# Performance work log

Hardware: AMD Instinct MI355X
Metric: run time of the kernel (lower is better)

The kernel has to match this reference:

```python
import jax, jax.numpy as jnp
import numpy as np

B, N, HID = 4, 16384, 512
H, M = 8, 32          # num_heads, num_slices
D = HID // H          # head_dim = 64


def setup_inputs() -> dict:
    key = jax.random.key(0)
    ks = jax.random.split(key, 8)
    std = 0.02
    return {
        "x": jax.random.normal(ks[0], (B, N, HID), jnp.float32),
        # Linear weights stored as [in, out] (y = x @ W + b)
        "wkv_w": jax.random.normal(ks[1], (HID, 2 * HID), jnp.float32) * std,
        "wkv_b": jnp.zeros((2 * HID,), jnp.float32),
        "wtq": jax.random.normal(ks[2], (H, M, D), jnp.float32) * std,
        "alpha": jnp.ones((H,), jnp.float32),
        "qkv_w": jax.random.normal(ks[3], (HID, 3 * HID), jnp.float32) * std,
        "out_w": jax.random.normal(ks[4], (HID, HID), jnp.float32) * std,
        "out_b": jnp.zeros((HID,), jnp.float32),
    }


def _split_heads(t):  # [b, n, h*d] -> [b, h, n, d]
    b, n, _ = t.shape
    return t.reshape(b, n, H, D).transpose(0, 2, 1, 3)


def _mha(q, k, v):
    scale = q.shape[-1] ** -0.5
    dots = jnp.einsum('bhqd,bhkd->bhqk', q, k) * scale
    attn = jax.nn.softmax(dots, axis=-1)
    out = jnp.einsum('bhqk,bhkd->bhqd', attn, v)
    return out, attn


def reference(x, wkv_w, wkv_b, wtq, alpha, qkv_w, out_w, out_b):
    kv = x @ wkv_w + wkv_b                      # [b, n, 2*hid]
    xk, xv = kv[..., :HID], kv[..., HID:]
    xk = _split_heads(xk)                       # [b, h, n, d]
    xv = _split_heads(xv)

    # slot/slice cross-attention: softmax over the slice axis m (axis=-2)
    slice_scores = jnp.einsum('hmd,bhnd->bhmn', wtq, xk)
    slice_weights = jax.nn.softmax(slice_scores * alpha[None, :, None, None], axis=-2)
    slice_token = jnp.einsum('bhmn,bhnd->bhmd', slice_weights, xv)
    slice_token = slice_token / (slice_weights.sum(axis=-1, keepdims=True) + 1e-5)
    slice_token = slice_token.transpose(0, 2, 1, 3).reshape(B, M, HID)  # b m (h d)

    # small inner MHA over the m=32 slices
    qkv = slice_token @ qkv_w                   # [b, m, 3*hid]
    q_t = _split_heads(qkv[..., :HID])
    k_t = _split_heads(qkv[..., HID:2 * HID])
    v_t = _split_heads(qkv[..., 2 * HID:])
    out_token, attn_weights = _mha(q_t, k_t, v_t)

    # scatter slice outputs back to n positions
    out = jnp.einsum('bhmd,bhmn->bhnd', out_token, slice_weights)
    out = out.transpose(0, 2, 1, 3).reshape(B, N, HID)  # b n (h d)
    out = out @ out_w + out_b
    return out, slice_weights, alpha, jnp.zeros((H, M), jnp.float32), attn_weights
```

## Files before the change

### kernel.cpp

```cpp
#include <hip/hip_runtime.h>

#define B_ 4
#define N_ 16384
#define HID_ 512
#define H_ 8
#define M_ 32
#define D_ 64

typedef __attribute__((ext_vector_type(8))) short short8;
typedef __attribute__((ext_vector_type(4))) float f32x4;

__device__ __forceinline__ short f2bf(float f) {
    unsigned u = __float_as_uint(f);
    u += 0x7fffu + ((u >> 16) & 1u);
    return (short)(u >> 16);
}
__device__ __forceinline__ float bf2f(short s) {
    return __uint_as_float(((unsigned)(unsigned short)s) << 16);
}
__device__ __forceinline__ unsigned pack2(float a, float b) {
    return (unsigned)(unsigned short)f2bf(a) | ((unsigned)(unsigned short)f2bf(b) << 16);
}
__device__ __forceinline__ void gl_lds16(const short* g, short* l) {
    __builtin_amdgcn_global_load_lds((const __attribute__((address_space(1))) unsigned*)g,
                                     (__attribute__((address_space(3))) unsigned*)l, 16, 0, 0);
}

__global__ void k_misc(const float* __restrict__ alpha, float* __restrict__ a_out,
                       float* __restrict__ z_out, const float* __restrict__ wtq,
                       short* __restrict__ wtq_bf) {
    int i = blockIdx.x * 256 + threadIdx.x;
    wtq_bf[i] = f2bf(wtq[i]);
    if (blockIdx.x == 0) {
        int t = threadIdx.x;
        if (t < H_) a_out[t] = alpha[t];
        z_out[t] = 0.f;
    }
}

__global__ void k_cvt(const float* __restrict__ src, short* __restrict__ dst) {
    int i = blockIdx.x * 256 + threadIdx.x;
    const f32x4* s = (const f32x4*)(src) + (size_t)i * 2;
    f32x4 a = s[0], b = s[1];
    short8 o;
    o[0] = f2bf(a[0]); o[1] = f2bf(a[1]); o[2] = f2bf(a[2]); o[3] = f2bf(a[3]);
    o[4] = f2bf(b[0]); o[5] = f2bf(b[1]); o[6] = f2bf(b[2]); o[7] = f2bf(b[3]);
    ((short8*)dst)[i] = o;
}

__global__ __launch_bounds__(256)
void k_wt(const float* __restrict__ w, short* __restrict__ wt) {
    __shared__ float ls[64][65];
    const int t = threadIdx.x;
    const int n0 = blockIdx.x * 64, k0 = blockIdx.y * 64;
#pragma unroll
    for (int p = 0; p < 16; ++p) {
        int idx = p * 256 + t;
        int kk = idx >> 6, nn = idx & 63;
        ls[kk][nn] = w[(size_t)(k0 + kk) * 1024 + n0 + nn];
    }
    __syncthreads();
#pragma unroll
    for (int p = 0; p < 16; ++p) {
        int idx = p * 256 + t;
        int nn = idx >> 6, kk = idx & 63;
        wt[(size_t)(n0 + nn) * 512 + k0 + kk] = f2bf(ls[kk][nn]);
    }
}

template <bool OUT_BF16>
__global__ __launch_bounds__(256, 2)
void mfma_gemm(const short* __restrict__ A, const short* __restrict__ Bt,
               const float* __restrict__ bias, void* __restrict__ Cv,
               int K, int Ncols, int b_stride, int rows_per_b, int lgx) {
    __shared__ short As[128 * 32];
    __shared__ short Bs[128 * 32];
    const int t = threadIdx.x;
    const int nwg = gridDim.x * gridDim.y;
    int id = blockIdx.y * gridDim.x + blockIdx.x;
    id = (id & 7) * (nwg >> 3) + (id >> 3);
    const int col0 = (id & ((1 << lgx) - 1)) * 128;
    const int row0 = (id >> lgx) * 128;
    const short* Bblk = Bt;
    if (b_stride) Bblk += (size_t)(row0 / rows_per_b) * (size_t)b_stride;

    const int r_a = t >> 2;
    const int c_a = (t & 3) << 3;
    const short* Ap = A + (size_t)(row0 + r_a) * K + c_a;
    const short* Bp = Bblk + (size_t)(col0 + r_a) * K + c_a;
    short* As0 = &As[t << 3];
    short* Bs0 = &Bs[t << 3];
    const size_t rowskip = (size_t)64 * K;

    const int w = t >> 6;
    const int L = t & 63;
    const int wm = (w >> 1) << 6;
    const int wn = (w & 1) << 6;
    const int lm = L & 15;
    const int lq = L >> 4;

    f32x4 acc[4][4];
#pragma unroll
    for (int i = 0; i < 4; ++i)
#pragma unroll
        for (int j = 0; j < 4; ++j) acc[i][j] = (f32x4){0.f, 0.f, 0.f, 0.f};

    for (int k0 = 0; k0 < K; k0 += 32) {
        gl_lds16(Ap + k0, As0);
        gl_lds16(Ap + k0 + rowskip, As0 + 2048);
        gl_lds16(Bp + k0, Bs0);
        gl_lds16(Bp + k0 + rowskip, Bs0 + 2048);
        __syncthreads();
        short8 af[4], bfr[4];
#pragma unroll
        for (int i = 0; i < 4; ++i)
            af[i] = *(const short8*)&As[((wm + (i << 4) + lm) << 5) + (lq << 3)];
#pragma unroll
        for (int j = 0; j < 4; ++j)
            bfr[j] = *(const short8*)&Bs[((wn + (j << 4) + lm) << 5) + (lq << 3)];
#pragma unroll
        for (int i = 0; i < 4; ++i)
#pragma unroll
            for (int j = 0; j < 4; ++j)
                acc[i][j] = __builtin_amdgcn_mfma_f32_16x16x32_bf16(af[i], bfr[j], acc[i][j], 0, 0, 0);
        __syncthreads();
    }
#pragma unroll
    for (int i = 0; i < 4; ++i) {
#pragma unroll
        for (int j = 0; j < 4; ++j) {
            const int gr = row0 + wm + (i << 4) + (lq << 2);
            const int gc = col0 + wn + (j << 4) + lm;
            const float bv = bias[gc];
#pragma unroll
            for (int r = 0; r < 4; ++r) {
                float v = acc[i][j][r] + bv;
                if constexpr (OUT_BF16)
                    ((short*)Cv)[(size_t)(gr + r) * Ncols + gc] = f2bf(v);
                else
                    ((float*)Cv)[(size_t)(gr + r) * Ncols + gc] = v;
            }
        }
    }
}

__global__ __launch_bounds__(256, 4)
void k_score(const short* __restrict__ kv, const short* __restrict__ wtq_bf,
             const float* __restrict__ alpha, float* __restrict__ sw_out,
             short* __restrict__ swT, float* __restrict__ pws) {
    __shared__ __attribute__((aligned(16))) short wT_s[M_ * 256];
    const int t = threadIdx.x;
    const int bx = blockIdx.x;
    const int chunk = bx & 63;
    const int h = (bx >> 6) & 7;
    const int b = bx >> 9;
    const int w = t >> 6;
    const int L = t & 63;
    const int lm = L & 15;
    const int g = L >> 4;
    const int n0 = chunk * 256;
    const size_t rowb = (size_t)(b * N_ + n0);
    const float al = alpha[h];

    short8 bq[2][2];
    const short* wq = wtq_bf + h * (M_ * D_);
#pragma unroll
    for (int mt = 0; mt < 2; ++mt)
#pragma unroll
        for (int ks = 0; ks < 2; ++ks)
            bq[mt][ks] = *(const short8*)(wq + (mt * 16 + lm) * 64 + ks * 32 + g * 8);

    f32x4 s[4][2];
#pragma unroll
    for (int nt = 0; nt < 4; ++nt)
#pragma unroll
        for (int mt = 0; mt < 2; ++mt) s[nt][mt] = (f32x4){0.f, 0.f, 0.f, 0.f};
#pragma unroll
    for (int ks = 0; ks < 2; ++ks) {
        short8 aq[4];
#pragma unroll
        for (int nt = 0; nt < 4; ++nt)
            aq[nt] = *(const short8*)(kv + (rowb + w * 64 + nt * 16 + lm) * 1024 +
                                      h * 64 + ks * 32 + g * 8);
#pragma unroll
        for (int nt = 0; nt < 4; ++nt)
#pragma unroll
            for (int mt = 0; mt < 2; ++mt)
                s[nt][mt] = __builtin_amdgcn_mfma_f32_16x16x32_bf16(aq[nt], bq[mt][ks], s[nt][mt], 0, 0, 0);
    }

#pragma unroll
    for (int nt = 0; nt < 4; ++nt)
#pragma unroll
        for (int r = 0; r < 4; ++r) {
            float v0 = s[nt][0][r] * al, v1 = s[nt][1][r] * al;
            float mx = fmaxf(v0, v1);
#pragma unroll
            for (int d2 = 1; d2 < 16; d2 <<= 1) mx = fmaxf(mx, __shfl_xor(mx, d2));
            float e0 = __expf(v0 - mx), e1 = __expf(v1 - mx);
            float sm = e0 + e1;
#pragma unroll
            for (int d2 = 1; d2 < 16; d2 <<= 1) sm += __shfl_xor(sm, d2);
            float inv = 1.f / sm;
            s[nt][0][r] = e0 * inv;
            s[nt][1][r] = e1 * inv;
        }

    float ws0 = 0.f, ws1 = 0.f;
#pragma unroll
    for (int nt = 0; nt < 4; ++nt) {
        const int nn = w * 64 + nt * 16 + g * 4;
#pragma unroll
        for (int mt = 0; mt < 2; ++mt) {
            const int m = mt * 16 + lm;
            *(f32x4*)(sw_out + ((size_t)((b * 8 + h) * 32 + m)) * N_ + n0 + nn) = s[nt][mt];
            float w4 = s[nt][mt][0] + s[nt][mt][1] + s[nt][mt][2] + s[nt][mt][3];
            if (mt == 0) ws0 += w4; else ws1 += w4;
            unsigned lo = pack2(s[nt][mt][0], s[nt][mt][1]);
            unsigned hi = pack2(s[nt][mt][2], s[nt][mt][3]);
            *(uint2*)(wT_s + m * 256 + (nn ^ ((m & 7) << 3))) = make_uint2(lo, hi);
        }
    }
    ws0 += __shfl_xor(ws0, 16); ws0 += __shfl_xor(ws0, 32);
    ws1 += __shfl_xor(ws1, 16); ws1 += __shfl_xor(ws1, 32);
    if (L < 16) {
        float* pw = pws + (((size_t)((b * 8 + h) * 64 + chunk)) * 4 + w) * 32;
        pw[lm] = ws0;
        pw[16 + lm] = ws1;
    }
    __syncthreads();

    unsigned pk[16];
#pragma unroll
    for (int mp = 0; mp < 16; ++mp) {
        unsigned a0 = (unsigned short)wT_s[(2 * mp) * 256 + (t ^ (((2 * mp) & 7) << 3))];
        unsigned a1 = (unsigned short)wT_s[(2 * mp + 1) * 256 + (t ^ (((2 * mp + 1) & 7) << 3))];
        pk[mp] = a0 | (a1 << 16);
    }
    short8* swtp = (short8*)(swT + (rowb + t) * 256 + h * 32);
#pragma unroll
    for (int q = 0; q < 4; ++q) {
        short8 v;
        v[0] = (short)(pk[4 * q] & 0xffff);     v[1] = (short)(pk[4 * q] >> 16);
        v[2] = (short)(pk[4 * q + 1] & 0xffff); v[3] = (short)(pk[4 * q + 1] >> 16);
        v[4] = (short)(pk[4 * q + 2] & 0xffff); v[5] = (short)(pk[4 * q + 2] >> 16);
        v[6] = (short)(pk[4 * q + 3] & 0xffff); v[7] = (short)(pk[4 * q + 3] >> 16);
        swtp[q] = v;
    }
}

__global__ __attribute__((amdgpu_flat_work_group_size(256, 256), amdgpu_waves_per_eu(3, 3)))
void k_wsum(const short* __restrict__ kv, const short* __restrict__ swT,
            float* __restrict__ pnum) {
    __shared__ __attribute__((aligned(16))) short wT_s[M_ * 256];
    __shared__ __attribute__((aligned(16))) short xvT_s[D_ * 256];
    const int t = threadIdx.x;
    const int bx = blockIdx.x;
    const int chunk = bx & 63;
    const int h = (bx >> 6) & 7;
    const int b = bx >> 9;
    const int w = t >> 6;
    const int L = t & 63;
    const int lm = L & 15;
    const int g = L >> 4;
    const int n0 = chunk * 256;
    const size_t rowb = (size_t)(b * N_ + n0);

    short8 xv8[8];
    const short8* xvp = (const short8*)(kv + (rowb + t) * 1024 + HID_ + h * 64);
#pragma unroll
    for (int i = 0; i < 8; ++i) xv8[i] = xvp[i];

    short8 sw4[4];
    const short8* swp = (const short8*)(swT + (rowb + t) * 256 + h * 32);
#pragma unroll
    for (int q = 0; q < 4; ++q) sw4[q] = swp[q];

#pragma unroll
    for (int q = 0; q < 4; ++q)
#pragma unroll
        for (int j = 0; j < 8; ++j) {
            const int m = q * 8 + j;
            wT_s[m * 256 + (t ^ ((m & 7) << 3))] = sw4[q][j];
        }

#pragma unroll
    for (int i = 0; i < 8; ++i)
#pragma unroll
        for (int j = 0; j < 8; ++j)
            xvT_s[(i * 8 + j) * 256 + (t ^ (j << 3))] = xv8[i][j];

    __syncthreads();

    const int dcol = w * 16 + lm;
    f32x4 acc2[2];
    acc2[0] = (f32x4){0.f, 0.f, 0.f, 0.f};
    acc2[1] = (f32x4){0.f, 0.f, 0.f, 0.f};
#pragma unroll
    for (int ks = 0; ks < 8; ++ks) {
        const int kb = ks * 32 + g * 8;
        short8 bv = *(const short8*)(xvT_s + dcol * 256 + (kb ^ ((lm & 7) << 3)));
#pragma unroll
        for (int mt = 0; mt < 2; ++mt) {
            const int m = mt * 16 + lm;
            short8 av = *(const short8*)(wT_s + m * 256 + (kb ^ ((lm & 7) << 3)));
            acc2[mt] = __builtin_amdgcn_mfma_f32_16x16x32_bf16(av, bv, acc2[mt], 0, 0, 0);
        }
    }

    float* pn = pnum + ((size_t)((b * 8 + h) * 64 + chunk)) * 2048;
#pragma unroll
    for (int mt = 0; mt < 2; ++mt)
#pragma unroll
        for (int r = 0; r < 4; ++r)
            pn[(mt * 16 + g * 4 + r) * 64 + dcol] = acc2[mt][r];
}

__global__ __launch_bounds__(256)
void k_reduce(const float* __restrict__ pnum, const float* __restrict__ pws,
              float* __restrict__ num, float* __restrict__ wsum) {
    const int bid = blockIdx.x, t = threadIdx.x;
    if (bid < 256) {
        int e = bid * 256 + t;
        int bh = e >> 11, md = e & 2047;
        const float* p = pnum + (size_t)bh * 64 * 2048 + md;
        float s = 0.f;
#pragma unroll 4
        for (int c = 0; c < 64; ++c) s += p[c * 2048];
        num[e] = s;
    } else {
        int e = (bid - 256) * 256 + t;
        int bh = e >> 5, m = e & 31;
        const float* p = pws + (size_t)bh * 64 * 4 * 32 + m;
        float s = 0.f;
#pragma unroll 4
        for (int cw = 0; cw < 256; ++cw) s += p[cw * 32];
        wsum[e] = s;
    }
}

__global__ __launch_bounds__(256, 2)
void k_qkv(const float* __restrict__ num, const float* __restrict__ wsum,
           const float* __restrict__ qkv_w, float* __restrict__ qkv) {
    __shared__ float st_s[512 * 32];
    const int t = threadIdx.x;
    const int b = blockIdx.y;
    for (int p = 0; p < 64; ++p) {
        int idx = p * 256 + t;
        int m = idx & 31, k = idx >> 5;
        int h = k >> 6, d = k & 63;
        float wsv = wsum[(b * H_ + h) * M_ + m];
        st_s[k * 32 + m] = num[((size_t)(b * H_ + h) * M_ + m) * 64 + d] / (wsv + 1e-5f);
    }
    __syncthreads();
    const int m = t >> 3;
    const int c0 = blockIdx.x * 64 + (t & 7) * 8;
    float acc[8] = {};
    for (int k = 0; k < 512; ++k) {
        float sv = st_s[k * 32 + m];
        const f32x4* wp = (const f32x4*)(qkv_w + (size_t)k * 1536 + c0);
        f32x4 w0 = wp[0], w1 = wp[1];
        acc[0] += sv * w0[0]; acc[1] += sv * w0[1]; acc[2] += sv * w0[2]; acc[3] += sv * w0[3];
        acc[4] += sv * w1[0]; acc[5] += sv * w1[1]; acc[6] += sv * w1[2]; acc[7] += sv * w1[3];
    }
    float* dst = qkv + (size_t)(b * M_ + m) * 1536 + c0;
#pragma unroll
    for (int i = 0; i < 8; ++i) dst[i] = acc[i];
}

__global__ __launch_bounds__(256)
void k_mha(const float* __restrict__ qkv, float* __restrict__ attn_out,
           float* __restrict__ ot) {
    __shared__ float q_s[32 * 65], k_s[32 * 65], v_s[32 * 65];
    __shared__ float s_s[32 * 33], p_s[32 * 33];
    const int bx = blockIdx.x;
    const int b = bx >> 3, h = bx & 7;
    const int t = threadIdx.x;
    for (int p = 0; p < 8; ++p) {
        int idx = p * 256 + t;
        int m = idx >> 6, d = idx & 63;
        size_t base = (size_t)(b * M_ + m) * 1536 + h * 64 + d;
        q_s[m * 65 + d] = qkv[base];
        k_s[m * 65 + d] = qkv[base + 512];
        v_s[m * 65 + d] = qkv[base + 1024];
    }
    __syncthreads();
    for (int p = 0; p < 4; ++p) {
        int c = p * 256 + t;
        int m = c >> 5, mm = c & 31;
        float a = 0.f;
#pragma unroll
        for (int d = 0; d < 64; ++d) a += q_s[m * 65 + d] * k_s[mm * 65 + d];
        s_s[m * 33 + mm] = a * 0.125f;
    }
    __syncthreads();
    if (t < 32) {
        float mx = -1e30f;
        for (int mm = 0; mm < 32; ++mm) mx = fmaxf(mx, s_s[t * 33 + mm]);
        float sum = 0.f;
        for (int mm = 0; mm < 32; ++mm) {
            float e = __expf(s_s[t * 33 + mm] - mx);
            p_s[t * 33 + mm] = e;
            sum += e;
        }
        float inv = 1.f / sum;
        for (int mm = 0; mm < 32; ++mm) {
            float av = p_s[t * 33 + mm] * inv;
            p_s[t * 33 + mm] = av;
            attn_out[((size_t)(b * H_ + h) * M_ + t) * M_ + mm] = av;
        }
    }
    __syncthreads();
    const int m = t >> 3, d0 = (t & 7) * 8;
    float acc[8] = {};
    for (int mm = 0; mm < 32; ++mm) {
        float av = p_s[m * 33 + mm];
#pragma unroll
        for (int j = 0; j < 8; ++j) acc[j] += av * v_s[mm * 65 + d0 + j];
    }
    float* dst = ot + ((size_t)(b * H_ + h) * M_ + m) * 64 + d0;
#pragma unroll
    for (int j = 0; j < 8; ++j) dst[j] = acc[j];
}

__global__ __launch_bounds__(256)
void k_p(const float* __restrict__ ot, const float* __restrict__ out_w,
         short* __restrict__ Pt) {
    __shared__ float ot_s[32 * 65];
    const int bh = blockIdx.y;
    const int b = bh >> 3, h = bh & 7;
    const int t = threadIdx.x;
    for (int p = 0; p < 8; ++p) {
        int idx = p * 256 + t;
        int m = idx >> 6, d = idx & 63;
        ot_s[m * 65 + d] = ot[(size_t)bh * (M_ * 64) + idx];
    }
    __syncthreads();
    const int j = blockIdx.x * 128 + (t & 127);
    const int mh = (t >> 7) * 16;
    float acc[16] = {};
    for (int d = 0; d < 64; ++d) {
        float ow = out_w[(size_t)(h * 64 + d) * HID_ + j];
#pragma unroll
        for (int i = 0; i < 16; ++i) acc[i] += ot_s[(mh + i) * 65 + d] * ow;
    }
    short* dst = Pt + ((size_t)b * HID_ + j) * (H_ * M_) + h * M_ + mh;
#pragma unroll
    for (int i = 0; i < 16; i += 2) *(unsigned*)(dst + i) = pack2(acc[i], acc[i + 1]);
}

extern "C" void kernel_launch(void* const* d_in, const int* in_sizes, int n_in,
                              void* d_out, int out_size, void* d_ws, size_t ws_size,
                              hipStream_t stream) {
    const float* x     = (const float*)d_in[0];
    const float* wkv_w = (const float*)d_in[1];
    const float* wkv_b = (const float*)d_in[2];
    const float* wtq   = (const float*)d_in[3];
    const float* alpha = (const float*)d_in[4];
    const float* qkv_w = (const float*)d_in[5];
    const float* out_w = (const float*)d_in[6];
    const float* out_b = (const float*)d_in[7];

    float* out       = (float*)d_out;
    float* sw_out    = out + (size_t)B_ * N_ * HID_;
    float* alpha_out = sw_out + (size_t)B_ * H_ * M_ * N_;
    float* zeros_out = alpha_out + H_;
    float* attn_out  = zeros_out + H_ * M_;

    short* x_bf = (short*)sw_out;
    float* pnum = out;
    float* pws  = out + 4194304;

    char* ws = (char*)d_ws;
    short* kv   = (short*)(ws);
    short* swT  = (short*)(ws + 134217728);
    short* wkvT = (short*)(ws + 167772160);
    short* Pt   = (short*)(ws + 168820736);
    float* num  = (float*)(ws + 169869312);
    float* wsum = (float*)(ws + 170131456);
    float* qkvb = (float*)(ws + 170135552);
    float* ot   = (float*)(ws + 170921984);
    short* wtq_bf = (short*)(ws + 170921984);

    k_misc<<<64, 256, 0, stream>>>(alpha, alpha_out, zeros_out, wtq, wtq_bf);
    k_cvt<<<16384, 256, 0, stream>>>(x, x_bf);
    k_wt<<<dim3(16, 8), 256, 0, stream>>>(wkv_w, wkvT);
    mfma_gemm<true><<<dim3(8, 512), 256, 0, stream>>>(
        x_bf, wkvT, wkv_b, (void*)kv, 512, 1024, 0, 1 << 30, 3);
    k_score<<<2048, 256, 0, stream>>>(kv, wtq_bf, alpha, sw_out, swT, pws);
    k_wsum<<<2048, 256, 0, stream>>>(kv, swT, pnum);
    k_reduce<<<260, 256, 0, stream>>>(pnum, pws, num, wsum);
    k_qkv<<<dim3(24, 4), 256, 0, stream>>>(num, wsum, qkv_w, qkvb);
    k_mha<<<32, 256, 0, stream>>>(qkvb, attn_out, ot);
    k_p<<<dim3(4, 32), 256, 0, stream>>>(ot, out_w, Pt);
    mfma_gemm<false><<<dim3(4, 512), 256, 0, stream>>>(
        swT, Pt, out_b, (void*)out, 256, 512, 131072, 16384, 2);
}
```

Baseline: 556.1 us.

## Double GEMM K-tile to 64 with XOR-swizzled LDS layout and setprio around MFMAs

Widens the GEMM K step from 32 to 64, so each iteration loads twice as much data and there are half as many barriers. The LDS tiles use an XOR swizzle on 16-byte chunks, with the global-to-LDS load addresses permuted to match, to avoid bank conflicts on the wider rows. It also raises wave priority around the MFMA block in the slice-score kernel. The cost is double the shared memory per block, which may reduce occupancy under the 2-blocks launch bound.

```diff
diff --git a/kernel.cpp b/kernel.cpp
--- a/kernel.cpp
+++ b/kernel.cpp
@@ -73,8 +73,8 @@
 void mfma_gemm(const short* __restrict__ A, const short* __restrict__ Bt,
                const float* __restrict__ bias, void* __restrict__ Cv,
                int K, int Ncols, int b_stride, int rows_per_b, int lgx) {
-    __shared__ short As[128 * 32];
-    __shared__ short Bs[128 * 32];
+    __shared__ short As[128 * 64];
+    __shared__ short Bs[128 * 64];
     const int t = threadIdx.x;
     const int nwg = gridDim.x * gridDim.y;
     int id = blockIdx.y * gridDim.x + blockIdx.x;
@@ -84,13 +84,14 @@
     const short* Bblk = Bt;
     if (b_stride) Bblk += (size_t)(row0 / rows_per_b) * (size_t)b_stride;
 
-    const int r_a = t >> 2;
-    const int c_a = (t & 3) << 3;
-    const short* Ap = A + (size_t)(row0 + r_a) * K + c_a;
-    const short* Bp = Bblk + (size_t)(col0 + r_a) * K + c_a;
-    short* As0 = &As[t << 3];
-    short* Bs0 = &Bs[t << 3];
-    const size_t rowskip = (size_t)64 * K;
+    int srow[4], scol[4];
+#pragma unroll
+    for (int c = 0; c < 4; ++c) {
+        int lin = (c * 256 + t) * 16;
+        int logo = lin ^ (((lin >> 7) & 7) << 4);
+        srow[c] = logo >> 7;
+        scol[c] = (logo & 127) >> 1;
+    }
 
     const int w = t >> 6;
     const int L = t & 63;
@@ -105,24 +106,36 @@
 #pragma unroll
         for (int j = 0; j < 4; ++j) acc[i][j] = (f32x4){0.f, 0.f, 0.f, 0.f};
 
-    for (int k0 = 0; k0 < K; k0 += 32) {
-        gl_lds16(Ap + k0, As0);
-        gl_lds16(Ap + k0 + rowskip, As0 + 2048);
-        gl_lds16(Bp + k0, Bs0);
-        gl_lds16(Bp + k0 + rowskip, Bs0 + 2048);
+    for (int k0 = 0; k0 < K; k0 += 64) {
+#pragma unroll
+        for (int c = 0; c < 4; ++c) {
+            gl_lds16(A + (size_t)(row0 + srow[c]) * K + k0 + scol[c], &As[(c * 256 + t) * 8]);
+            gl_lds16(Bblk + (size_t)(col0 + srow[c]) * K + k0 + scol[c], &Bs[(c * 256 + t) * 8]);
+        }
         __syncthreads();
-        short8 af[4], bfr[4];
-#pragma unroll
-        for (int i = 0; i < 4; ++i)
-            af[i] = *(const short8*)&As[((wm + (i << 4) + lm) << 5) + (lq << 3)];
-#pragma unroll
-        for (int j = 0; j < 4; ++j)
-            bfr[j] = *(const short8*)&Bs[((wn + (j << 4) + lm) << 5) + (lq << 3)];
-#pragma unroll
-        for (int i = 0; i < 4; ++i)
-#pragma unroll
-            for (int j = 0; j < 4; ++j)
-                acc[i][j] = __builtin_amdgcn_mfma_f32_16x16x32_bf16(af[i], bfr[j], acc[i][j], 0, 0, 0);
+#pragma unroll
+        for (int ks = 0; ks < 2; ++ks) {
+            short8 af[4], bfr[4];
+#pragma unroll
+            for (int i = 0; i < 4; ++i) {
+                const int row = wm + (i << 4) + lm;
+                int pb = (row << 7) + (ks << 6) + (lq << 4);
+                pb ^= (row & 7) << 4;
+                af[i] = *(const short8*)&As[pb >> 1];
+            }
+#pragma unroll
+            for (int j = 0; j < 4; ++j) {
+                const int row = wn + (j << 4) + lm;
+                int pb = (row << 7) + (ks << 6) + (lq << 4);
+                pb ^= (row & 7) << 4;
+                bfr[j] = *(const short8*)&Bs[pb >> 1];
+            }
+#pragma unroll
+            for (int i = 0; i < 4; ++i)
+#pragma unroll
+                for (int j = 0; j < 4; ++j)
+                    acc[i][j] = __builtin_amdgcn_mfma_f32_16x16x32_bf16(af[i], bfr[j], acc[i][j], 0, 0, 0);
+        }
         __syncthreads();
     }
 #pragma unroll
@@ -182,11 +195,13 @@
         for (int nt = 0; nt < 4; ++nt)
             aq[nt] = *(const short8*)(kv + (rowb + w * 64 + nt * 16 + lm) * 1024 +
                                       h * 64 + ks * 32 + g * 8);
+        __builtin_amdgcn_s_setprio(1);
 #pragma unroll
         for (int nt = 0; nt < 4; ++nt)
 #pragma unroll
             for (int mt = 0; mt < 2; ++mt)
                 s[nt][mt] = __builtin_amdgcn_mfma_f32_16x16x32_bf16(aq[nt], bq[mt][ks], s[nt][mt], 0, 0, 0);
+        __builtin_amdgcn_s_setprio(0);
     }
 
 #pragma unroll
```

Measured after the change: 551.6 us. Within noise of the previous version (-0.8%).
